# Kernel optimization log

Hardware: AMD Instinct MI355X
Metric: run time of the kernel (lower is better)

The kernel has to match this reference:

```python
import jax, jax.numpy as jnp
import numpy as np

T, H, I, E, K = 1024, 2048, 1408, 8, 2  # tokens, hidden, moe_intermediate, n_experts, top_k

def setup_inputs() -> dict:
    key = jax.random.key(0)
    k0, k1, k2, k3 = jax.random.split(key, 4)
    def w(k, shape, fan_in):
        return jax.random.normal(k, shape, jnp.float32) / np.float32(np.sqrt(fan_in))
    return {
        "hidden_states": jax.random.normal(k0, (T, H), jnp.float32),
        "gate_w": w(k1, (H, E), H),      # router: LiteLinear(H -> E), no bias
        "w1": w(k2, (E, H, I), H),        # experts_w1 [E, H, I]
        "w2": w(k3, (E, I, H), I),        # experts_w2 [E, I, H]
    }

def reference(hidden_states, gate_w, w1, w2):
    # Router: logits -> softmax -> top-k expert probabilities (no renorm; Qwen2MoE norm_topk_prob=False)
    router_logits = hidden_states @ gate_w                      # [T, E]
    probs = jax.nn.softmax(router_logits, axis=-1)              # [T, E]
    topk_vals, topk_idx = jax.lax.top_k(probs, K)               # [T, K]
    # Dense combine weights: zero except at the top-k experts of each token
    combine = jnp.sum(jax.nn.one_hot(topk_idx, E, dtype=probs.dtype) * topk_vals[..., None], axis=1)  # [T, E]
    # Expert MLP per source: down(silu(x @ w1)) — note: no gate/up split in this repo's fused_moe weights
    h = jnp.einsum('th,ehi->tei', hidden_states, w1)            # [T, E, I]
    y = jnp.einsum('tei,eih->teh', jax.nn.silu(h), w2)          # [T, E, H]
    return jnp.einsum('te,teh->th', combine, y)                 # [T, H]
```

## Files before the change

kernel.cpp:

```cpp
#include <hip/hip_runtime.h>
#include <hip/hip_fp16.h>

#define T_TOK 1024
#define H_DIM 2048
#define I_DIM 1408
#define N_EXP 8
#define TOPK  2

using f16x8 = __attribute__((ext_vector_type(8))) _Float16;
using f32x4 = __attribute__((ext_vector_type(4))) float;

#define BM 128
#define BN 64
#define BK 64
#define NTHR 512

#define WS_COUNTS      0
#define WS_BASES       256
#define WS_CURSORS     512
#define WS_TOPK_E      768
#define WS_TOPK_W      (768 + 8192)
#define WS_TOK_OF_SLOT 17408
#define WS_W_OF_SLOT   29696
#define WS_HACT        43008
#define WS_NEEDED      (43008 + 8650752)

__global__ void k_router(const float* __restrict__ X, const float* __restrict__ GW,
                         int* __restrict__ counts, int* __restrict__ topk_e,
                         float* __restrict__ topk_w) {
    int t = (blockIdx.x * blockDim.x + threadIdx.x) >> 6;
    int lane = threadIdx.x & 63;
    if (t >= T_TOK) return;
    float acc[N_EXP];
#pragma unroll
    for (int e = 0; e < N_EXP; ++e) acc[e] = 0.f;
    const float* xrow = X + (size_t)t * H_DIM;
    for (int h = lane; h < H_DIM; h += 64) {
        float x = xrow[h];
        const float* g = GW + (size_t)h * N_EXP;
#pragma unroll
        for (int e = 0; e < N_EXP; ++e) acc[e] = fmaf(x, g[e], acc[e]);
    }
#pragma unroll
    for (int off = 32; off > 0; off >>= 1) {
#pragma unroll
        for (int e = 0; e < N_EXP; ++e) acc[e] += __shfl_xor(acc[e], off, 64);
    }
    if (lane == 0) {
        float m = acc[0];
#pragma unroll
        for (int e = 1; e < N_EXP; ++e) m = fmaxf(m, acc[e]);
        float ex[N_EXP], s = 0.f;
#pragma unroll
        for (int e = 0; e < N_EXP; ++e) { ex[e] = expf(acc[e] - m); s += ex[e]; }
        float inv = 1.f / s;
        int e1 = 0;
#pragma unroll
        for (int e = 1; e < N_EXP; ++e) if (ex[e] > ex[e1]) e1 = e;
        int e2 = (e1 == 0) ? 1 : 0;
#pragma unroll
        for (int e = 0; e < N_EXP; ++e) if (e != e1 && ex[e] > ex[e2]) e2 = e;
        topk_e[t * 2 + 0] = e1;
        topk_e[t * 2 + 1] = e2;
        topk_w[t * 2 + 0] = ex[e1] * inv;
        topk_w[t * 2 + 1] = ex[e2] * inv;
        atomicAdd(&counts[e1], 1);
        atomicAdd(&counts[e2], 1);
    }
}

__global__ void k_prefix(const int* __restrict__ counts, int* __restrict__ bases,
                         int* __restrict__ cursors) {
    if (threadIdx.x == 0) {
        int b = 0;
        for (int e = 0; e < N_EXP; ++e) {
            bases[e] = b;
            b += ((counts[e] + BM - 1) / BM) * BM;
            cursors[e] = 0;
        }
    }
}

__global__ void k_scatter(const int* __restrict__ topk_e, const float* __restrict__ topk_w,
                          const int* __restrict__ bases, int* __restrict__ cursors,
                          int* __restrict__ tok_of_slot, float* __restrict__ w_of_slot) {
    int t = blockIdx.x * blockDim.x + threadIdx.x;
    if (t >= T_TOK) return;
    for (int j = 0; j < TOPK; ++j) {
        int e = topk_e[t * 2 + j];
        int pos = atomicAdd(&cursors[e], 1);
        int slot = bases[e] + pos;
        tok_of_slot[slot] = t;
        w_of_slot[slot] = topk_w[t * 2 + j];
    }
}

__global__ __launch_bounds__(NTHR, 4) void k_gemm1(
    const float* __restrict__ X, const float* __restrict__ W1,
    const int* __restrict__ counts, const int* __restrict__ bases,
    const int* __restrict__ tok_of_slot, const float* __restrict__ w_of_slot,
    _Float16* __restrict__ hact) {
    __shared__ _Float16 As[2][BM][BK];
    __shared__ _Float16 Bs[2][BN][BK];

    const int e = blockIdx.z;
    const int cnt = counts[e];
    const int m0 = blockIdx.y * BM;
    if (m0 >= cnt) return;
    const int base = bases[e];
    const int n0 = blockIdx.x * BN;
    const int tid = threadIdx.x;

    const int ar = tid >> 2;
    const int ac2 = (tid & 3) * 2;
    const int r_eff = min(ar, cnt - m0 - 1);
    const float* arow = X + (size_t)tok_of_slot[base + m0 + r_eff] * H_DIM + (tid & 3) * 16;

    const int bn = tid & 63;
    const int bc = tid >> 6;
    const float* bcol = W1 + (size_t)e * H_DIM * I_DIM + (size_t)(bc * 8) * I_DIM + n0 + bn;

    const int wid = tid >> 6, lane = tid & 63;
    const int wm = (wid >> 1) * 32, wn = (wid & 1) * 32;
    const int rsel = lane & 15, kq = lane >> 4;

    f32x4 acc[2][2] = {};

    float4 aR0[4]; float bR0[8];
    float4 aR1[4]; float bR1[8];

#define LOAD1(aR, bR, k0)                                              \
    do {                                                               \
        aR[0] = *(const float4*)(arow + (k0));                         \
        aR[1] = *(const float4*)(arow + (k0) + 4);                     \
        aR[2] = *(const float4*)(arow + (k0) + 8);                     \
        aR[3] = *(const float4*)(arow + (k0) + 12);                    \
        const float* bp = bcol + (size_t)(k0) * I_DIM;                 \
        _Pragma("unroll") for (int j = 0; j < 8; ++j)                  \
            bR[j] = bp[(size_t)j * I_DIM];                             \
    } while (0)

#define STORE1(buf, aR, bR)                                            \
    do {                                                               \
        f16x8 p0, p1;                                                  \
        _Pragma("unroll") for (int j = 0; j < 4; ++j) {                \
            p0[j]     = (_Float16)aR[0][j];                            \
            p0[j + 4] = (_Float16)aR[1][j];                            \
            p1[j]     = (_Float16)aR[2][j];                            \
            p1[j + 4] = (_Float16)aR[3][j];                            \
        }                                                              \
        *(f16x8*)&As[buf][ar][((ac2) ^ (ar & 7)) * 8] = p0;            \
        *(f16x8*)&As[buf][ar][((ac2 + 1) ^ (ar & 7)) * 8] = p1;        \
        f16x8 q;                                                       \
        _Pragma("unroll") for (int j = 0; j < 8; ++j)                  \
            q[j] = (_Float16)bR[j];                                    \
        *(f16x8*)&Bs[buf][bn][(bc ^ (bn & 7)) * 8] = q;                \
    } while (0)

#define COMPUTE(buf)                                                   \
    do {                                                               \
        _Pragma("unroll") for (int ks = 0; ks < 2; ++ks) {             \
            f16x8 af[2], bf[2];                                        \
            _Pragma("unroll") for (int i = 0; i < 2; ++i) {            \
                int r = wm + i * 16 + rsel;                            \
                af[i] = *(const f16x8*)&As[buf][r][((kq + 4 * ks) ^ (r & 7)) * 8]; \
            }                                                          \
            _Pragma("unroll") for (int j = 0; j < 2; ++j) {            \
                int r = wn + j * 16 + rsel;                            \
                bf[j] = *(const f16x8*)&Bs[buf][r][((kq + 4 * ks) ^ (r & 7)) * 8]; \
            }                                                          \
            _Pragma("unroll") for (int i = 0; i < 2; ++i)              \
                _Pragma("unroll") for (int j = 0; j < 2; ++j)          \
                    acc[i][j] = __builtin_amdgcn_mfma_f32_16x16x32_f16(af[i], bf[j], acc[i][j], 0, 0, 0); \
        }                                                              \
    } while (0)

    const int KT = H_DIM / BK;
    LOAD1(aR0, bR0, 0);
    STORE1(0, aR0, bR0);
    LOAD1(aR0, bR0, BK);
    __syncthreads();
    for (int kt = 0; kt < KT; kt += 2) {
        if (kt + 2 < KT) LOAD1(aR1, bR1, (kt + 2) * BK);
        COMPUTE(0);
        if (kt + 1 < KT) STORE1(1, aR0, bR0);
        __syncthreads();
        if (kt + 3 < KT) LOAD1(aR0, bR0, (kt + 3) * BK);
        if (kt + 1 < KT) {
            COMPUTE(1);
            if (kt + 2 < KT) STORE1(0, aR1, bR1);
            __syncthreads();
        }
    }
#undef LOAD1
#undef STORE1
#undef COMPUTE

    const int rows = cnt - m0;
#pragma unroll
    for (int i = 0; i < 2; ++i) {
#pragma unroll
        for (int q = 0; q < 4; ++q) {
            int r = wm + i * 16 + kq * 4 + q;
            if (r < rows) {
                int slot = base + m0 + r;
                float w = w_of_slot[slot];
                _Float16* hrow = hact + (size_t)slot * I_DIM + n0;
#pragma unroll
                for (int j = 0; j < 2; ++j) {
                    float v = acc[i][j][q];
                    float s = v / (1.f + expf(-v)) * w;
                    hrow[wn + j * 16 + rsel] = (_Float16)s;
                }
            }
        }
    }
}

__global__ __launch_bounds__(NTHR, 4) void k_gemm2(
    const _Float16* __restrict__ hact, const float* __restrict__ W2,
    const int* __restrict__ counts, const int* __restrict__ bases,
    const int* __restrict__ tok_of_slot, float* __restrict__ out) {
    __shared__ _Float16 As[2][BM][BK];
    __shared__ _Float16 Bs[2][BN][BK];

    const int e = blockIdx.z;
    const int cnt = counts[e];
    const int m0 = blockIdx.y * BM;
    if (m0 >= cnt) return;
    const int base = bases[e];
    const int n0 = blockIdx.x * BN;
    const int tid = threadIdx.x;

    const int ar = tid >> 2;
    const int ac2 = (tid & 3) * 2;
    const int r_eff = min(ar, cnt - m0 - 1);
    const _Float16* arow = hact + (size_t)(base + m0 + r_eff) * I_DIM + (tid & 3) * 16;

    const int bn = tid & 63;
    const int bc = tid >> 6;
    const float* bcol = W2 + (size_t)e * I_DIM * H_DIM + (size_t)(bc * 8) * H_DIM + n0 + bn;

    const int wid = tid >> 6, lane = tid & 63;
    const int wm = (wid >> 1) * 32, wn = (wid & 1) * 32;
    const int rsel = lane & 15, kq = lane >> 4;

    f32x4 acc[2][2] = {};

    f16x8 aR0[2]; float bR0[8];
    f16x8 aR1[2]; float bR1[8];

#define LOAD2(aR, bR, k0)                                              \
    do {                                                               \
        aR[0] = *(const f16x8*)(arow + (k0));                          \
        aR[1] = *(const f16x8*)(arow + (k0) + 8);                      \
        const float* bp = bcol + (size_t)(k0) * H_DIM;                 \
        _Pragma("unroll") for (int j = 0; j < 8; ++j)                  \
            bR[j] = bp[(size_t)j * H_DIM];                             \
    } while (0)

#define STORE2(buf, aR, bR)                                            \
    do {                                                               \
        *(f16x8*)&As[buf][ar][((ac2) ^ (ar & 7)) * 8] = aR[0];         \
        *(f16x8*)&As[buf][ar][((ac2 + 1) ^ (ar & 7)) * 8] = aR[1];     \
        f16x8 q;                                                       \
        _Pragma("unroll") for (int j = 0; j < 8; ++j)                  \
            q[j] = (_Float16)bR[j];                                    \
        *(f16x8*)&Bs[buf][bn][(bc ^ (bn & 7)) * 8] = q;                \
    } while (0)

#define COMPUTE2(buf)                                                  \
    do {                                                               \
        _Pragma("unroll") for (int ks = 0; ks < 2; ++ks) {             \
            f16x8 af[2], bf[2];                                        \
            _Pragma("unroll") for (int i = 0; i < 2; ++i) {            \
                int r = wm + i * 16 + rsel;                            \
                af[i] = *(const f16x8*)&As[buf][r][((kq + 4 * ks) ^ (r & 7)) * 8]; \
            }                                                          \
            _Pragma("unroll") for (int j = 0; j < 2; ++j) {            \
                int r = wn + j * 16 + rsel;                            \
                bf[j] = *(const f16x8*)&Bs[buf][r][((kq + 4 * ks) ^ (r & 7)) * 8]; \
            }                                                          \
            _Pragma("unroll") for (int i = 0; i < 2; ++i)              \
                _Pragma("unroll") for (int j = 0; j < 2; ++j)          \
                    acc[i][j] = __builtin_amdgcn_mfma_f32_16x16x32_f16(af[i], bf[j], acc[i][j], 0, 0, 0); \
        }                                                              \
    } while (0)

    const int KT = I_DIM / BK;
    LOAD2(aR0, bR0, 0);
    STORE2(0, aR0, bR0);
    LOAD2(aR0, bR0, BK);
    __syncthreads();
    for (int kt = 0; kt < KT; kt += 2) {
        if (kt + 2 < KT) LOAD2(aR1, bR1, (kt + 2) * BK);
        COMPUTE2(0);
        if (kt + 1 < KT) STORE2(1, aR0, bR0);
        __syncthreads();
        if (kt + 3 < KT) LOAD2(aR0, bR0, (kt + 3) * BK);
        if (kt + 1 < KT) {
            COMPUTE2(1);
            if (kt + 2 < KT) STORE2(0, aR1, bR1);
            __syncthreads();
        }
    }
#undef LOAD2
#undef STORE2
#undef COMPUTE2

    const int rows = cnt - m0;
#pragma unroll
    for (int i = 0; i < 2; ++i) {
#pragma unroll
        for (int q = 0; q < 4; ++q) {
            int r = wm + i * 16 + kq * 4 + q;
            if (r < rows) {
                int slot = base + m0 + r;
                int tok = tok_of_slot[slot];
                float* orow = out + (size_t)tok * H_DIM + n0;
#pragma unroll
                for (int j = 0; j < 2; ++j)
                    atomicAdd(&orow[wn + j * 16 + rsel], acc[i][j][q]);
            }
        }
    }
}

extern "C" void kernel_launch(void* const* d_in, const int* in_sizes, int n_in,
                              void* d_out, int out_size, void* d_ws, size_t ws_size,
                              hipStream_t stream) {
    const float* X  = (const float*)d_in[0];
    const float* GW = (const float*)d_in[1];
    const float* W1 = (const float*)d_in[2];
    const float* W2 = (const float*)d_in[3];
    float* out = (float*)d_out;
    char* ws = (char*)d_ws;
    if (ws_size < (size_t)WS_NEEDED) return;

    int*   counts      = (int*)(ws + WS_COUNTS);
    int*   bases       = (int*)(ws + WS_BASES);
    int*   cursors     = (int*)(ws + WS_CURSORS);
    int*   topk_e      = (int*)(ws + WS_TOPK_E);
    float* topk_w      = (float*)(ws + WS_TOPK_W);
    int*   tok_of_slot = (int*)(ws + WS_TOK_OF_SLOT);
    float* w_of_slot   = (float*)(ws + WS_W_OF_SLOT);
    _Float16* hact     = (_Float16*)(ws + WS_HACT);

    hipMemsetAsync(counts, 0, N_EXP * sizeof(int), stream);
    k_router<<<T_TOK / 4, 256, 0, stream>>>(X, GW, counts, topk_e, topk_w);
    k_prefix<<<1, 64, 0, stream>>>(counts, bases, cursors);
    k_scatter<<<T_TOK / 256, 256, 0, stream>>>(topk_e, topk_w, bases, cursors,
                                               tok_of_slot, w_of_slot);
    hipMemsetAsync(out, 0, (size_t)T_TOK * H_DIM * sizeof(float), stream);
    k_gemm1<<<dim3(I_DIM / BN, T_TOK / BM, N_EXP), NTHR, 0, stream>>>(
        X, W1, counts, bases, tok_of_slot, w_of_slot, hact);
    k_gemm2<<<dim3(H_DIM / BN, T_TOK / BM, N_EXP), NTHR, 0, stream>>>(
        hact, W2, counts, bases, tok_of_slot, out);
}
```

Baseline: 166.1 us.

## Deepen register prefetch, shrink tiles, and remap blocks so XCDs share expert weights

Both expert GEMMs now use 64-row tiles with 256 threads and keep four K-tiles of global loads in flight in registers instead of two. B loads become float2 per thread. The grid is flattened to 1D and remapped so that blocks sharing an expert and N column land on the same XCD, which should improve L2 reuse of weights. Deeper prefetch costs more registers (launch bounds go to 3 waves), and smaller M tiles mean weight tiles are re-read more often across M blocks.

```diff
diff --git a/kernel.cpp b/kernel.cpp
--- a/kernel.cpp
+++ b/kernel.cpp
@@ -10,10 +10,10 @@
 using f16x8 = __attribute__((ext_vector_type(8))) _Float16;
 using f32x4 = __attribute__((ext_vector_type(4))) float;
 
-#define BM 128
+#define BM 64
 #define BN 64
 #define BK 64
-#define NTHR 512
+#define NTHR 256
 
 #define WS_COUNTS      0
 #define WS_BASES       256
@@ -95,7 +95,26 @@
     }
 }
 
-__global__ __launch_bounds__(NTHR, 4) void k_gemm1(
+
+#define G_COMPUTE(buf)                                                          \
+    do {                                                                        \
+        _Pragma("unroll") for (int ks = 0; ks < 2; ++ks) {                      \
+            f16x8 af[2], bf[2];                                                 \
+            _Pragma("unroll") for (int ii = 0; ii < 2; ++ii) {                  \
+                int r = wm + ii * 16 + rsel;                                    \
+                af[ii] = *(const f16x8*)&As[buf][r][((kq + 4 * ks) ^ (r & 7)) * 8]; \
+            }                                                                   \
+            _Pragma("unroll") for (int jj = 0; jj < 2; ++jj) {                  \
+                int r = wn + jj * 16 + rsel;                                    \
+                bf[jj] = *(const f16x8*)&Bs[buf][r][((kq + 4 * ks) ^ (r & 7)) * 8]; \
+            }                                                                   \
+            _Pragma("unroll") for (int ii = 0; ii < 2; ++ii)                    \
+                _Pragma("unroll") for (int jj = 0; jj < 2; ++jj)                \
+                    acc[ii][jj] = __builtin_amdgcn_mfma_f32_16x16x32_f16(af[ii], bf[jj], acc[ii][jj], 0, 0, 0); \
+        }                                                                       \
+    } while (0)
+
+__global__ __launch_bounds__(NTHR, 3) void k_gemm1(
     const float* __restrict__ X, const float* __restrict__ W1,
     const int* __restrict__ counts, const int* __restrict__ bases,
     const int* __restrict__ tok_of_slot, const float* __restrict__ w_of_slot,
@@ -103,22 +122,28 @@
     __shared__ _Float16 As[2][BM][BK];
     __shared__ _Float16 Bs[2][BN][BK];
 
-    const int e = blockIdx.z;
+    const int bi = blockIdx.x;
+    const int xcd = bi & 7;
+    const int kk = bi >> 3;
+    const int mblk = kk & 15;
+    const int pair = xcd + 8 * (kk >> 4);
+    const int e = pair & 7;
+    const int n = pair >> 3;
     const int cnt = counts[e];
-    const int m0 = blockIdx.y * BM;
+    const int m0 = mblk * BM;
     if (m0 >= cnt) return;
     const int base = bases[e];
-    const int n0 = blockIdx.x * BN;
+    const int n0 = n * BN;
     const int tid = threadIdx.x;
 
     const int ar = tid >> 2;
-    const int ac2 = (tid & 3) * 2;
+    const int as0 = (tid & 3) * 2;
     const int r_eff = min(ar, cnt - m0 - 1);
     const float* arow = X + (size_t)tok_of_slot[base + m0 + r_eff] * H_DIM + (tid & 3) * 16;
 
-    const int bn = tid & 63;
-    const int bc = tid >> 6;
-    const float* bcol = W1 + (size_t)e * H_DIM * I_DIM + (size_t)(bc * 8) * I_DIM + n0 + bn;
+    const int bn2 = (tid & 31) * 2;
+    const int bc = tid >> 5;
+    const float* bcol = W1 + (size_t)e * (H_DIM * I_DIM) + (size_t)(bc * 8) * I_DIM + n0 + bn2;
 
     const int wid = tid >> 6, lane = tid & 63;
     const int wm = (wid >> 1) * 32, wn = (wid & 1) * 32;
@@ -126,120 +151,116 @@
 
     f32x4 acc[2][2] = {};
 
-    float4 aR0[4]; float bR0[8];
-    float4 aR1[4]; float bR1[8];
-
-#define LOAD1(aR, bR, k0)                                              \
-    do {                                                               \
-        aR[0] = *(const float4*)(arow + (k0));                         \
-        aR[1] = *(const float4*)(arow + (k0) + 4);                     \
-        aR[2] = *(const float4*)(arow + (k0) + 8);                     \
-        aR[3] = *(const float4*)(arow + (k0) + 12);                    \
-        const float* bp = bcol + (size_t)(k0) * I_DIM;                 \
-        _Pragma("unroll") for (int j = 0; j < 8; ++j)                  \
-            bR[j] = bp[(size_t)j * I_DIM];                             \
-    } while (0)
-
-#define STORE1(buf, aR, bR)                                            \
-    do {                                                               \
-        f16x8 p0, p1;                                                  \
-        _Pragma("unroll") for (int j = 0; j < 4; ++j) {                \
-            p0[j]     = (_Float16)aR[0][j];                            \
-            p0[j + 4] = (_Float16)aR[1][j];                            \
-            p1[j]     = (_Float16)aR[2][j];                            \
-            p1[j + 4] = (_Float16)aR[3][j];                            \
-        }                                                              \
-        *(f16x8*)&As[buf][ar][((ac2) ^ (ar & 7)) * 8] = p0;            \
-        *(f16x8*)&As[buf][ar][((ac2 + 1) ^ (ar & 7)) * 8] = p1;        \
-        f16x8 q;                                                       \
-        _Pragma("unroll") for (int j = 0; j < 8; ++j)                  \
-            q[j] = (_Float16)bR[j];                                    \
-        *(f16x8*)&Bs[buf][bn][(bc ^ (bn & 7)) * 8] = q;                \
-    } while (0)
-
-#define COMPUTE(buf)                                                   \
-    do {                                                               \
-        _Pragma("unroll") for (int ks = 0; ks < 2; ++ks) {             \
-            f16x8 af[2], bf[2];                                        \
-            _Pragma("unroll") for (int i = 0; i < 2; ++i) {            \
-                int r = wm + i * 16 + rsel;                            \
-                af[i] = *(const f16x8*)&As[buf][r][((kq + 4 * ks) ^ (r & 7)) * 8]; \
-            }                                                          \
-            _Pragma("unroll") for (int j = 0; j < 2; ++j) {            \
-                int r = wn + j * 16 + rsel;                            \
-                bf[j] = *(const f16x8*)&Bs[buf][r][((kq + 4 * ks) ^ (r & 7)) * 8]; \
-            }                                                          \
-            _Pragma("unroll") for (int i = 0; i < 2; ++i)              \
-                _Pragma("unroll") for (int j = 0; j < 2; ++j)          \
-                    acc[i][j] = __builtin_amdgcn_mfma_f32_16x16x32_f16(af[i], bf[j], acc[i][j], 0, 0, 0); \
-        }                                                              \
-    } while (0)
-
-    const int KT = H_DIM / BK;
-    LOAD1(aR0, bR0, 0);
-    STORE1(0, aR0, bR0);
-    LOAD1(aR0, bR0, BK);
+    float4 aS0[4], aS1[4], aS2[4], aS3[4];
+    float2 bS0[8], bS1[8], bS2[8], bS3[8];
+
+#define G1_LOAD(aS, bS, t)                                         \
+    do {                                                           \
+        const float* ap = arow + (t) * BK;                         \
+        aS[0] = *(const float4*)(ap);                              \
+        aS[1] = *(const float4*)(ap + 4);                          \
+        aS[2] = *(const float4*)(ap + 8);                          \
+        aS[3] = *(const float4*)(ap + 12);                         \
+        const float* bp = bcol + (size_t)((t) * BK) * I_DIM;       \
+        _Pragma("unroll") for (int j = 0; j < 8; ++j)              \
+            bS[j] = *(const float2*)(bp + (size_t)j * I_DIM);      \
+    } while (0)
+
+#define G1_STORE(buf, aS, bS)                                      \
+    do {                                                           \
+        f16x8 p0, p1;                                              \
+        _Pragma("unroll") for (int c = 0; c < 4; ++c) {            \
+            p0[c] = (_Float16)aS[0][c]; p0[c + 4] = (_Float16)aS[1][c]; \
+            p1[c] = (_Float16)aS[2][c]; p1[c + 4] = (_Float16)aS[3][c]; \
+        }                                                          \
+        *(f16x8*)&As[buf][ar][((as0) ^ (ar & 7)) * 8] = p0;        \
+        *(f16x8*)&As[buf][ar][((as0 + 1) ^ (ar & 7)) * 8] = p1;    \
+        f16x8 q0, q1;                                              \
+        _Pragma("unroll") for (int j = 0; j < 8; ++j) {            \
+            q0[j] = (_Float16)bS[j].x; q1[j] = (_Float16)bS[j].y;  \
+        }                                                          \
+        *(f16x8*)&Bs[buf][bn2][(bc ^ (bn2 & 7)) * 8] = q0;         \
+        *(f16x8*)&Bs[buf][bn2 + 1][(bc ^ ((bn2 + 1) & 7)) * 8] = q1; \
+    } while (0)
+
+    constexpr int KT = H_DIM / BK;
+    constexpr int QUADS = (KT - 1) / 4;
+    constexpr int REM = (KT - 1) & 3;
+
+    G1_LOAD(aS0, bS0, 0);
+    G1_LOAD(aS1, bS1, 1);
+    G1_LOAD(aS2, bS2, 2);
+    G1_LOAD(aS3, bS3, 3);
+    G1_STORE(0, aS0, bS0);
     __syncthreads();
-    for (int kt = 0; kt < KT; kt += 2) {
-        if (kt + 2 < KT) LOAD1(aR1, bR1, (kt + 2) * BK);
-        COMPUTE(0);
-        if (kt + 1 < KT) STORE1(1, aR0, bR0);
-        __syncthreads();
-        if (kt + 3 < KT) LOAD1(aR0, bR0, (kt + 3) * BK);
-        if (kt + 1 < KT) {
-            COMPUTE(1);
-            if (kt + 2 < KT) STORE1(0, aR1, bR1);
-            __syncthreads();
-        }
-    }
-#undef LOAD1
-#undef STORE1
-#undef COMPUTE
+
+    int h = 0;
+    for (int q = 0; q < QUADS; ++q, h += 4) {
+        if (h + 4 < KT) G1_LOAD(aS0, bS0, h + 4);
+        G_COMPUTE(0); G1_STORE(1, aS1, bS1); __syncthreads();
+        if (h + 5 < KT) G1_LOAD(aS1, bS1, h + 5);
+        G_COMPUTE(1); G1_STORE(0, aS2, bS2); __syncthreads();
+        if (h + 6 < KT) G1_LOAD(aS2, bS2, h + 6);
+        G_COMPUTE(0); G1_STORE(1, aS3, bS3); __syncthreads();
+        if (h + 7 < KT) G1_LOAD(aS3, bS3, h + 7);
+        G_COMPUTE(1); G1_STORE(0, aS0, bS0); __syncthreads();
+    }
+    if constexpr (REM >= 1) { G_COMPUTE(0); G1_STORE(1, aS1, bS1); __syncthreads(); }
+    if constexpr (REM >= 2) { G_COMPUTE(1); G1_STORE(0, aS2, bS2); __syncthreads(); }
+    if constexpr (REM >= 3) { G_COMPUTE(0); G1_STORE(1, aS3, bS3); __syncthreads(); }
+    G_COMPUTE((KT - 1) & 1);
+#undef G1_LOAD
+#undef G1_STORE
 
     const int rows = cnt - m0;
 #pragma unroll
     for (int i = 0; i < 2; ++i) {
 #pragma unroll
-        for (int q = 0; q < 4; ++q) {
-            int r = wm + i * 16 + kq * 4 + q;
+        for (int rg = 0; rg < 4; ++rg) {
+            int r = wm + i * 16 + kq * 4 + rg;
             if (r < rows) {
                 int slot = base + m0 + r;
                 float w = w_of_slot[slot];
                 _Float16* hrow = hact + (size_t)slot * I_DIM + n0;
 #pragma unroll
                 for (int j = 0; j < 2; ++j) {
-                    float v = acc[i][j][q];
-                    float s = v / (1.f + expf(-v)) * w;
-                    hrow[wn + j * 16 + rsel] = (_Float16)s;
+                    float v = acc[i][j][rg];
+                    hrow[wn + j * 16 + rsel] = (_Float16)(v / (1.f + expf(-v)) * w);
                 }
             }
         }
     }
 }
 
-__global__ __launch_bounds__(NTHR, 4) void k_gemm2(
+__global__ __launch_bounds__(NTHR, 3) void k_gemm2(
     const _Float16* __restrict__ hact, const float* __restrict__ W2,
     const int* __restrict__ counts, const int* __restrict__ bases,
     const int* __restrict__ tok_of_slot, float* __restrict__ out) {
     __shared__ _Float16 As[2][BM][BK];
     __shared__ _Float16 Bs[2][BN][BK];
 
-    const int e = blockIdx.z;
+    const int bi = blockIdx.x;
+    const int xcd = bi & 7;
+    const int kk = bi >> 3;
+    const int mblk = kk & 15;
+    const int pair = xcd + 8 * (kk >> 4);
+    const int e = pair & 7;
+    const int n = pair >> 3;
     const int cnt = counts[e];
-    const int m0 = blockIdx.y * BM;
+    const int m0 = mblk * BM;
     if (m0 >= cnt) return;
     const int base = bases[e];
-    const int n0 = blockIdx.x * BN;
+    const int n0 = n * BN;
     const int tid = threadIdx.x;
 
     const int ar = tid >> 2;
-    const int ac2 = (tid & 3) * 2;
+    const int as0 = (tid & 3) * 2;
     const int r_eff = min(ar, cnt - m0 - 1);
     const _Float16* arow = hact + (size_t)(base + m0 + r_eff) * I_DIM + (tid & 3) * 16;
 
-    const int bn = tid & 63;
-    const int bc = tid >> 6;
-    const float* bcol = W2 + (size_t)e * I_DIM * H_DIM + (size_t)(bc * 8) * H_DIM + n0 + bn;
+    const int bn2 = (tid & 31) * 2;
+    const int bc = tid >> 5;
+    const float* bcol = W2 + (size_t)e * (I_DIM * H_DIM) + (size_t)(bc * 8) * H_DIM + n0 + bn2;
 
     const int wid = tid >> 6, lane = tid & 63;
     const int wm = (wid >> 1) * 32, wn = (wid & 1) * 32;
@@ -247,80 +268,73 @@
 
     f32x4 acc[2][2] = {};
 
-    f16x8 aR0[2]; float bR0[8];
-    f16x8 aR1[2]; float bR1[8];
-
-#define LOAD2(aR, bR, k0)                                              \
-    do {                                                               \
-        aR[0] = *(const f16x8*)(arow + (k0));                          \
-        aR[1] = *(const f16x8*)(arow + (k0) + 8);                      \
-        const float* bp = bcol + (size_t)(k0) * H_DIM;                 \
-        _Pragma("unroll") for (int j = 0; j < 8; ++j)                  \
-            bR[j] = bp[(size_t)j * H_DIM];                             \
-    } while (0)
-
-#define STORE2(buf, aR, bR)                                            \
-    do {                                                               \
-        *(f16x8*)&As[buf][ar][((ac2) ^ (ar & 7)) * 8] = aR[0];         \
-        *(f16x8*)&As[buf][ar][((ac2 + 1) ^ (ar & 7)) * 8] = aR[1];     \
-        f16x8 q;                                                       \
-        _Pragma("unroll") for (int j = 0; j < 8; ++j)                  \
-            q[j] = (_Float16)bR[j];                                    \
-        *(f16x8*)&Bs[buf][bn][(bc ^ (bn & 7)) * 8] = q;                \
-    } while (0)
-
-#define COMPUTE2(buf)                                                  \
-    do {                                                               \
-        _Pragma("unroll") for (int ks = 0; ks < 2; ++ks) {             \
-            f16x8 af[2], bf[2];                                        \
-            _Pragma("unroll") for (int i = 0; i < 2; ++i) {            \
-                int r = wm + i * 16 + rsel;                            \
-                af[i] = *(const f16x8*)&As[buf][r][((kq + 4 * ks) ^ (r & 7)) * 8]; \
-            }                                                          \
-            _Pragma("unroll") for (int j = 0; j < 2; ++j) {            \
-                int r = wn + j * 16 + rsel;                            \
-                bf[j] = *(const f16x8*)&Bs[buf][r][((kq + 4 * ks) ^ (r & 7)) * 8]; \
-            }                                                          \
-            _Pragma("unroll") for (int i = 0; i < 2; ++i)              \
-                _Pragma("unroll") for (int j = 0; j < 2; ++j)          \
-                    acc[i][j] = __builtin_amdgcn_mfma_f32_16x16x32_f16(af[i], bf[j], acc[i][j], 0, 0, 0); \
-        }                                                              \
-    } while (0)
-
-    const int KT = I_DIM / BK;
-    LOAD2(aR0, bR0, 0);
-    STORE2(0, aR0, bR0);
-    LOAD2(aR0, bR0, BK);
+    f16x8 aS0[2], aS1[2], aS2[2], aS3[2];
+    float2 bS0[8], bS1[8], bS2[8], bS3[8];
+
+#define G2_LOAD(aS, bS, t)                                         \
+    do {                                                           \
+        const _Float16* ap = arow + (t) * BK;                      \
+        aS[0] = *(const f16x8*)(ap);                               \
+        aS[1] = *(const f16x8*)(ap + 8);                           \
+        const float* bp = bcol + (size_t)((t) * BK) * H_DIM;       \
+        _Pragma("unroll") for (int j = 0; j < 8; ++j)              \
+            bS[j] = *(const float2*)(bp + (size_t)j * H_DIM);      \
+    } while (0)
+
+#define G2_STORE(buf, aS, bS)                                      \
+    do {                                                           \
+        *(f16x8*)&As[buf][ar][((as0) ^ (ar & 7)) * 8] = aS[0];     \
+        *(f16x8*)&As[buf][ar][((as0 + 1) ^ (ar & 7)) * 8] = aS[1]; \
+        f16x8 q0, q1;                                              \
+        _Pragma("unroll") for (int j = 0; j < 8; ++j) {            \
+            q0[j] = (_Float16)bS[j].x; q1[j] = (_Float16)bS[j].y;  \
+        }                                                          \
+        *(f16x8*)&Bs[buf][bn2][(bc ^ (bn2 & 7)) * 8] = q0;         \
+        *(f16x8*)&Bs[buf][bn2 + 1][(bc ^ ((bn2 + 1) & 7)) * 8] = q1; \
+    } while (0)
+
+    constexpr int KT = I_DIM / BK;
+    constexpr int QUADS = (KT - 1) / 4;
+    constexpr int REM = (KT - 1) & 3;
+
+    G2_LOAD(aS0, bS0, 0);
+    G2_LOAD(aS1, bS1, 1);
+    G2_LOAD(aS2, bS2, 2);
+    G2_LOAD(aS3, bS3, 3);
+    G2_STORE(0, aS0, bS0);
     __syncthreads();
-    for (int kt = 0; kt < KT; kt += 2) {
-        if (kt + 2 < KT) LOAD2(aR1, bR1, (kt + 2) * BK);
-        COMPUTE2(0);
-        if (kt + 1 < KT) STORE2(1, aR0, bR0);
-        __syncthreads();
-        if (kt + 3 < KT) LOAD2(aR0, bR0, (kt + 3) * BK);
-        if (kt + 1 < KT) {
-            COMPUTE2(1);
-            if (kt + 2 < KT) STORE2(0, aR1, bR1);
-            __syncthreads();
-        }
-    }
-#undef LOAD2
-#undef STORE2
-#undef COMPUTE2
+
+    int h = 0;
+    for (int q = 0; q < QUADS; ++q, h += 4) {
+        if (h + 4 < KT) G2_LOAD(aS0, bS0, h + 4);
+        G_COMPUTE(0); G2_STORE(1, aS1, bS1); __syncthreads();
+        if (h + 5 < KT) G2_LOAD(aS1, bS1, h + 5);
+        G_COMPUTE(1); G2_STORE(0, aS2, bS2); __syncthreads();
+        if (h + 6 < KT) G2_LOAD(aS2, bS2, h + 6);
+        G_COMPUTE(0); G2_STORE(1, aS3, bS3); __syncthreads();
+        if (h + 7 < KT) G2_LOAD(aS3, bS3, h + 7);
+        G_COMPUTE(1); G2_STORE(0, aS0, bS0); __syncthreads();
+    }
+    if constexpr (REM >= 1) { G_COMPUTE(0); G2_STORE(1, aS1, bS1); __syncthreads(); }
+    if constexpr (REM >= 2) { G_COMPUTE(1); G2_STORE(0, aS2, bS2); __syncthreads(); }
+    if constexpr (REM >= 3) { G_COMPUTE(0); G2_STORE(1, aS3, bS3); __syncthreads(); }
+    G_COMPUTE((KT - 1) & 1);
+#undef G2_LOAD
+#undef G2_STORE
 
     const int rows = cnt - m0;
 #pragma unroll
     for (int i = 0; i < 2; ++i) {
 #pragma unroll
-        for (int q = 0; q < 4; ++q) {
-            int r = wm + i * 16 + kq * 4 + q;
+        for (int rg = 0; rg < 4; ++rg) {
+            int r = wm + i * 16 + kq * 4 + rg;
             if (r < rows) {
                 int slot = base + m0 + r;
                 int tok = tok_of_slot[slot];
                 float* orow = out + (size_t)tok * H_DIM + n0;
 #pragma unroll
                 for (int j = 0; j < 2; ++j)
-                    atomicAdd(&orow[wn + j * 16 + rsel], acc[i][j][q]);
+                    atomicAdd(&orow[wn + j * 16 + rsel], acc[i][j][rg]);
             }
         }
     }
@@ -352,8 +366,8 @@
     k_scatter<<<T_TOK / 256, 256, 0, stream>>>(topk_e, topk_w, bases, cursors,
                                                tok_of_slot, w_of_slot);
     hipMemsetAsync(out, 0, (size_t)T_TOK * H_DIM * sizeof(float), stream);
-    k_gemm1<<<dim3(I_DIM / BN, T_TOK / BM, N_EXP), NTHR, 0, stream>>>(
+    k_gemm1<<<8 * 22 * 16, NTHR, 0, stream>>>(
         X, W1, counts, bases, tok_of_slot, w_of_slot, hact);
-    k_gemm2<<<dim3(H_DIM / BN, T_TOK / BM, N_EXP), NTHR, 0, stream>>>(
+    k_gemm2<<<8 * 32 * 16, NTHR, 0, stream>>>(
         hact, W2, counts, bases, tok_of_slot, out);
 }
```

New measurement: 301.8 us. 1.82x slower.
